# Optimization experiments

Measured on AMD Instinct MI355X. Metric: run time of the kernel, lower is better.

Reference implementation:

```python
import jax, jax.numpy as jnp
import numpy as np
from jax import lax

B, H, W, C = 16, 256, 256, 1
LOC_C = 31            # channels out of localization network
BN_EPS = 1e-3         # Keras BatchNormalization default epsilon
NEG_SLOPE = 0.1       # LeakyReLU slope


def _conv_relu(x, k, b):
    y = lax.conv_general_dilated(x, k, (1, 1), 'SAME',
                                 dimension_numbers=('NHWC', 'HWIO', 'NHWC'))
    return jax.nn.relu(y + b)


def _maxpool2(x):
    return lax.reduce_window(x, -jnp.inf, lax.max, (1, 2, 2, 1), (1, 2, 2, 1), 'VALID')


def _resize_nearest(x, out_h, out_w):
    # tf.image.resize(..., method='nearest') with half-pixel centers
    b, h, w, c = x.shape
    ih = jnp.floor((jnp.arange(out_h) + 0.5) * h / out_h).astype(jnp.int32)
    iw = jnp.floor((jnp.arange(out_w) + 0.5) * w / out_w).astype(jnp.int32)
    return x[:, ih][:, :, iw]


def _generate_grid(theta, height, width):
    # base grid in [-1, 1], x varies along width, y along height
    xs = jnp.arange(width, dtype=jnp.float32) / (width - 1) * 2.0 - 1.0
    ys = jnp.arange(height, dtype=jnp.float32) / (height - 1) * 2.0 - 1.0
    gx, gy = jnp.meshgrid(xs, ys)                      # (H, W)
    grid = jnp.stack([gx, gy], axis=-1).reshape(height * width, 2)  # (HW, 2)
    th = theta.reshape(-1, 2, 3)
    A = th[:, :, :2]                                   # (B, 2, 2)
    t = th[:, :, 2]                                    # (B, 2)
    # NOTE: source does grid @ A (not A @ grid) -- replicate exactly
    tg = jnp.einsum('nc,bcd->bnd', grid, A) + t[:, None, :]
    return tg.reshape(-1, height, width, 2)


def _sampler(img, grid):
    b, h, w, c = img.shape
    x = 0.5 * ((grid[..., 0] + 1.0) * (w - 1))
    y = 0.5 * ((grid[..., 1] + 1.0) * (h - 1))
    x0 = jnp.floor(x); x1 = x0 + 1.0
    y0 = jnp.floor(y); y1 = y0 + 1.0
    x0 = jnp.clip(x0, 0.0, w - 1.0); x1 = jnp.clip(x1, 0.0, w - 1.0)
    y0 = jnp.clip(y0, 0.0, h - 1.0); y1 = jnp.clip(y1, 0.0, h - 1.0)
    wa = (x1 - x) * (y1 - y)
    wb = (x1 - x) * (y - y0)
    wc = (x - x0) * (y1 - y)
    wd = (x - x0) * (y - y0)
    xi0 = x0.astype(jnp.int32); xi1 = x1.astype(jnp.int32)
    yi0 = y0.astype(jnp.int32); yi1 = y1.astype(jnp.int32)
    img_flat = img.reshape(b, h * w, c)

    def gather(yi, xi):
        idx = (yi * w + xi).reshape(b, h * w, 1)       # (B, HW, 1)
        return jnp.take_along_axis(img_flat, idx, axis=1).reshape(b, h, w, c)

    Ia = gather(yi0, xi0)
    Ib = gather(yi1, xi0)
    Ic = gather(yi0, xi1)
    Id = gather(yi1, xi1)
    return (wa[..., None] * Ia + wb[..., None] * Ib
            + wc[..., None] * Ic + wd[..., None] * Id)


def setup_inputs() -> dict:
    key = jax.random.key(0)
    ks = jax.random.split(key, 16)
    s = 0.05
    feat = (H // 8) * (W // 8) * LOC_C  # 31744 flattened localization features
    return {
        'x': jax.random.normal(ks[0], (B, H, W, C), jnp.float32),
        'conv1_k': jax.random.normal(ks[1], (3, 3, C, 8), jnp.float32) * s,
        'conv1_b': jnp.zeros((8,), jnp.float32),
        'conv2_k': jax.random.normal(ks[2], (3, 3, 8, 16), jnp.float32) * s,
        'conv2_b': jnp.zeros((16,), jnp.float32),
        'conv3_k': jax.random.normal(ks[3], (3, 3, 16, LOC_C), jnp.float32) * s,
        'conv3_b': jnp.zeros((LOC_C,), jnp.float32),
        'bn_gamma': 1.0 + 0.1 * jax.random.normal(ks[4], (feat,), jnp.float32),
        'bn_beta': 0.1 * jax.random.normal(ks[5], (feat,), jnp.float32),
        'bn_mean': jnp.zeros((feat,), jnp.float32),
        'bn_var': jnp.ones((feat,), jnp.float32),
        'd1_k': jax.random.normal(ks[6], (feat, 64), jnp.float32) * 0.01,
        'd1_b': jnp.zeros((64,), jnp.float32),
        'd2_k': jax.random.normal(ks[7], (64, 96), jnp.float32) * s,
        'd2_b': jnp.zeros((96,), jnp.float32),
        'd3_k': jax.random.normal(ks[8], (96, 6), jnp.float32) * 0.01,
        'd3_b': jnp.array([1, 0, 0, 0, 1, 0], jnp.float32),
    }


def reference(x, conv1_k, conv1_b, conv2_k, conv2_b, conv3_k, conv3_b,
              bn_gamma, bn_beta, bn_mean, bn_var,
              d1_k, d1_b, d2_k, d2_b, d3_k, d3_b):
    # localization network: (conv-relu, pool) x3 -> (B, H/8, W/8, 31)
    xi = _maxpool2(_conv_relu(x, conv1_k, conv1_b))
    xi = _maxpool2(_conv_relu(xi, conv2_k, conv2_b))
    x_intermediate = _maxpool2(_conv_relu(xi, conv3_k, conv3_b))
    # transformation parameter network (BN in inference mode, dropout = identity)
    f = x_intermediate.reshape(x.shape[0], -1)
    f = (f - bn_mean) * jax.lax.rsqrt(bn_var + BN_EPS) * bn_gamma + bn_beta
    f = jax.nn.relu(f @ d1_k + d1_b)
    f = jax.nn.relu(f @ d2_k + d2_b)
    theta = f @ d3_k + d3_b                            # (B, 6)
    grid = _generate_grid(theta, H, W)                 # (B, H, W, 2)
    loc_up = _resize_nearest(x_intermediate, H, W)     # (B, H, W, 31)
    xc = jnp.concatenate([x, loc_up], axis=-1)         # (B, H, W, 32)
    out = _sampler(xc, grid)
    return jnp.where(out >= 0, out, NEG_SLOPE * out)
```

## Files before the change

### kernel.cpp

```cpp
#include <hip/hip_runtime.h>


#define NEG_SLOPE 0.1f
#define BN_EPS 1e-3f

typedef float vfloat4 __attribute__((ext_vector_type(4)));

__device__ __forceinline__ void fma4v(float pv, float4 wq, float* __restrict__ acc) {
    acc[0] = fmaf(pv, wq.x, acc[0]);
    acc[1] = fmaf(pv, wq.y, acc[1]);
    acc[2] = fmaf(pv, wq.z, acc[2]);
    acc[3] = fmaf(pv, wq.w, acc[3]);
}

__global__ __launch_bounds__(256) void st_conv1(const float* __restrict__ x,
                                                const float* __restrict__ w,
                                                const float* __restrict__ bias,
                                                float* __restrict__ Ap,
                                                float* __restrict__ Bp) {
    int idx = blockIdx.x * 256 + threadIdx.x;
    int px = idx & 127, py = (idx >> 7) & 127, b = idx >> 14;
    const float* xb = x + b * 65536;
    int iy0 = 2 * py - 1, ix0 = 2 * px - 1;
    float p[16];
#pragma unroll
    for (int r = 0; r < 4; ++r) {
        int iy = iy0 + r;
        bool oky = (iy >= 0) && (iy < 256);
#pragma unroll
        for (int cc = 0; cc < 4; ++cc) {
            int ix = ix0 + cc;
            bool ok = oky && (ix >= 0) && (ix < 256);
            p[r * 4 + cc] = ok ? xb[iy * 256 + ix] : 0.0f;
        }
    }
    float m[8];
#pragma unroll
    for (int co = 0; co < 8; ++co) m[co] = -1e30f;
#pragma unroll
    for (int oy = 0; oy < 2; ++oy)
#pragma unroll
        for (int ox = 0; ox < 2; ++ox) {
            float acc[8];
#pragma unroll
            for (int co = 0; co < 8; ++co) acc[co] = 0.0f;
#pragma unroll
            for (int ky = 0; ky < 3; ++ky)
#pragma unroll
                for (int kx = 0; kx < 3; ++kx) {
                    float pv = p[(oy + ky) * 4 + (ox + kx)];
                    const float* wr = w + (ky * 3 + kx) * 8;
#pragma unroll
                    for (int co = 0; co < 8; ++co)
                        acc[co] = fmaf(pv, wr[co], acc[co]);
                }
#pragma unroll
            for (int co = 0; co < 8; ++co) m[co] = fmaxf(m[co], acc[co]);
        }
    float4 o0, o1;
    float r0 = m[0] + bias[0], r1 = m[1] + bias[1], r2 = m[2] + bias[2], r3 = m[3] + bias[3];
    float r4 = m[4] + bias[4], r5 = m[5] + bias[5], r6 = m[6] + bias[6], r7 = m[7] + bias[7];
    o0.x = r0 > 0.f ? r0 : 0.f; o0.y = r1 > 0.f ? r1 : 0.f;
    o0.z = r2 > 0.f ? r2 : 0.f; o0.w = r3 > 0.f ? r3 : 0.f;
    o1.x = r4 > 0.f ? r4 : 0.f; o1.y = r5 > 0.f ? r5 : 0.f;
    o1.z = r6 > 0.f ? r6 : 0.f; o1.w = r7 > 0.f ? r7 : 0.f;
    float* o = Ap + ((b * 130 + py + 1) * 130 + (px + 1)) * 8;
    *(float4*)o = o0;
    *(float4*)(o + 4) = o1;

    const float4 z4 = {0.f, 0.f, 0.f, 0.f};
    if (idx < 8256) {
        int bb = idx / 516, t = idx - bb * 516;
        int iy, ix;
        if (t < 130)      { iy = 0;       ix = t; }
        else if (t < 260) { iy = 129;     ix = t - 130; }
        else if (t < 388) { iy = t - 259; ix = 0; }
        else              { iy = t - 387; ix = 129; }
        float* d = Ap + ((bb * 130 + iy) * 130 + ix) * 8;
        *(float4*)d = z4; *(float4*)(d + 4) = z4;
    } else if (idx < 12416) {
        int r = idx - 8256;
        int bb = r / 260, t = r - bb * 260;
        int iy, ix;
        if (t < 66)       { iy = 0;       ix = t; }
        else if (t < 132) { iy = 65;      ix = t - 66; }
        else if (t < 196) { iy = t - 131; ix = 0; }
        else              { iy = t - 195; ix = 65; }
        float* d = Bp + ((bb * 66 + iy) * 66 + ix) * 16;
        *(float4*)d = z4; *(float4*)(d + 4) = z4;
        *(float4*)(d + 8) = z4; *(float4*)(d + 12) = z4;
    }
}

__global__ __launch_bounds__(256) void st_conv2(const float* __restrict__ Ap,
                                                const float* __restrict__ w,
                                                const float* __restrict__ bias,
                                                float* __restrict__ Bp) {
    __shared__ __align__(16) float wlds[1152];
    int t = threadIdx.x;
    for (int i = t; i < 1152; i += 256) wlds[i] = w[i];
    __syncthreads();
    int lane = t & 63;
    int wv = __builtin_amdgcn_readfirstlane(t >> 6);
    int cobase = wv * 4;
    int pixel = blockIdx.x * 64 + lane;
    int px = pixel & 63, py = (pixel >> 6) & 63, b = pixel >> 12;
    const float* Ab = Ap + b * 135200;
    int rowbase = (2 * py) * 130 + 2 * px;
    float acc[4][4];
#pragma unroll
    for (int pos = 0; pos < 4; ++pos)
#pragma unroll
        for (int c = 0; c < 4; ++c) acc[pos][c] = 0.0f;

#pragma unroll
    for (int ciq = 0; ciq < 2; ++ciq) {
        float ps[64];
#pragma unroll
        for (int r = 0; r < 4; ++r)
#pragma unroll
            for (int cc = 0; cc < 4; ++cc) {
                float4 v = *(const float4*)(Ab + (rowbase + r * 130 + cc) * 8 + ciq * 4);
                int cell = r * 4 + cc;
                ps[cell * 4 + 0] = v.x; ps[cell * 4 + 1] = v.y;
                ps[cell * 4 + 2] = v.z; ps[cell * 4 + 3] = v.w;
            }
#pragma unroll
        for (int ky = 0; ky < 3; ++ky)
#pragma unroll
            for (int kx = 0; kx < 3; ++kx) {
                int tap = ky * 3 + kx;
#pragma unroll
                for (int comp = 0; comp < 4; ++comp) {
                    float4 wq = *(const float4*)&wlds[((tap * 8 + ciq * 4 + comp) << 4) + cobase];
#pragma unroll
                    for (int oy = 0; oy < 2; ++oy)
#pragma unroll
                        for (int ox = 0; ox < 2; ++ox) {
                            float pv = ps[((oy + ky) * 4 + (ox + kx)) * 4 + comp];
                            fma4v(pv, wq, acc[oy * 2 + ox]);
                        }
                }
            }
    }
    float4 o;
    float* oc = (float*)&o;
#pragma unroll
    for (int c = 0; c < 4; ++c) {
        float m = fmaxf(fmaxf(acc[0][c], acc[1][c]), fmaxf(acc[2][c], acc[3][c]));
        m += bias[cobase + c];
        oc[c] = m > 0.0f ? m : 0.0f;
    }
    *(float4*)(Bp + ((b * 66 + py + 1) * 66 + (px + 1)) * 16 + cobase) = o;
}

__global__ __launch_bounds__(256) void st_conv3p(const float* __restrict__ Bp,
                                                 const float* __restrict__ w,
                                                 const float* __restrict__ bias,
                                                 const float* __restrict__ gamma,
                                                 const float* __restrict__ beta,
                                                 const float* __restrict__ mean,
                                                 const float* __restrict__ var,
                                                 float* __restrict__ xip,
                                                 float* __restrict__ fprime) {
    __shared__ __align__(16) float wlds[9 * 16 * 32];
    int t = threadIdx.x;
    for (int i = t; i < 4464; i += 256) {
        int tapci = i / 31;
        int co = i - tapci * 31;
        wlds[(tapci << 5) + co] = w[i];
    }
    __syncthreads();
    int lane = t & 63;
    int wv = __builtin_amdgcn_readfirstlane(t >> 6);
    int quad = blockIdx.y * 4 + wv;
    int cobase = quad * 4;
    if (cobase > 27) cobase = 27;
    int pixel = blockIdx.x * 64 + lane;
    int b = pixel >> 10;
    int cell = pixel & 1023;
    int ppy = cell >> 5, ppx = cell & 31;
    const float* Bb = Bp + b * 69696;
    int rowbase = (2 * ppy) * 66 + 2 * ppx;
    float acc[4][4];
#pragma unroll
    for (int pos = 0; pos < 4; ++pos)
#pragma unroll
        for (int c = 0; c < 4; ++c) acc[pos][c] = 0.0f;

#pragma unroll 2
    for (int ciq = 0; ciq < 4; ++ciq) {
        float ps[64];
#pragma unroll
        for (int r = 0; r < 4; ++r)
#pragma unroll
            for (int cc = 0; cc < 4; ++cc) {
                float4 v = *(const float4*)(Bb + (rowbase + r * 66 + cc) * 16 + ciq * 4);
                int cell2 = r * 4 + cc;
                ps[cell2 * 4 + 0] = v.x; ps[cell2 * 4 + 1] = v.y;
                ps[cell2 * 4 + 2] = v.z; ps[cell2 * 4 + 3] = v.w;
            }
#pragma unroll
        for (int ky = 0; ky < 3; ++ky)
#pragma unroll
            for (int kx = 0; kx < 3; ++kx) {
                int tap = ky * 3 + kx;
#pragma unroll
                for (int comp = 0; comp < 4; ++comp) {
                    float4 wq = *(const float4*)&wlds[((tap * 16 + ciq * 4 + comp) << 5) + cobase];
#pragma unroll
                    for (int oy = 0; oy < 2; ++oy)
#pragma unroll
                        for (int ox = 0; ox < 2; ++ox) {
                            float pv = ps[((oy + ky) * 4 + (ox + kx)) * 4 + comp];
                            fma4v(pv, wq, acc[oy * 2 + ox]);
                        }
                }
            }
    }
    float* xcell = xip + (b << 15) + (cell << 5) + 1 + cobase;
#pragma unroll
    for (int c = 0; c < 4; ++c) {
        float m = fmaxf(fmaxf(acc[0][c], acc[1][c]), fmaxf(acc[2][c], acc[3][c]));
        m += bias[cobase + c];
        float v = m > 0.0f ? m : 0.0f;
        xcell[c] = v;
        int j = cell * 31 + cobase + c;
        float sc = gamma[j] * rsqrtf(var[j] + BN_EPS);
        fprime[j * 16 + b] = (v - mean[j]) * sc + beta[j];
    }
}

__global__ __launch_bounds__(256) void st_d1(const float* __restrict__ fp,
                                             const float* __restrict__ k1,
                                             float* __restrict__ partial) {
    int t = threadIdx.x, s = blockIdx.x;
    int o = t & 63;
    int sub = t >> 6;
    int subu = __builtin_amdgcn_readfirstlane(sub);
    int j0 = s * 64 + subu * 16;
    float acc[16];
#pragma unroll
    for (int b = 0; b < 16; ++b) acc[b] = 0.0f;
#pragma unroll 4
    for (int jj = 0; jj < 16; ++jj) {
        int j = j0 + jj;
        float kv = k1[j * 64 + o];
        const float* fpj = fp + j * 16;
#pragma unroll
        for (int b = 0; b < 16; ++b)
            acc[b] = fmaf(fpj[b], kv, acc[b]);
    }
    __shared__ float red[4][16][64];
#pragma unroll
    for (int b = 0; b < 16; ++b) red[sub][b][o] = acc[b];
    __syncthreads();
    if (sub == 0) {
#pragma unroll
        for (int b = 0; b < 16; ++b) {
            float v = red[0][b][o] + red[1][b][o] + red[2][b][o] + red[3][b][o];
            partial[(s * 64 + o) * 16 + b] = v;
        }
    }
}

__global__ __launch_bounds__(256) void st_d1b(const float* __restrict__ partial,
                                              const float* __restrict__ bias,
                                              float* __restrict__ h1) {
    int gid = blockIdx.x * 256 + threadIdx.x;
    int o = gid >> 4, b = gid & 15;
    float s = 0.0f;
#pragma unroll 8
    for (int sl = 0; sl < 496; ++sl) s += partial[(sl * 64 + o) * 16 + b];
    s += bias[o];
    h1[b * 64 + o] = s > 0.0f ? s : 0.0f;
}

__global__ __launch_bounds__(128) void st_theta(const float* __restrict__ h1,
                                                const float* __restrict__ k2,
                                                const float* __restrict__ b2,
                                                const float* __restrict__ k3,
                                                const float* __restrict__ b3,
                                                float* __restrict__ theta) {
    int b = blockIdx.x, t = threadIdx.x;
    __shared__ float h2[96];
    if (t < 96) {
        float s = b2[t];
        for (int i = 0; i < 64; ++i) s = fmaf(h1[b * 64 + i], k2[i * 96 + t], s);
        h2[t] = s > 0.0f ? s : 0.0f;
    }
    __syncthreads();
    if (t < 6) {
        float s = b3[t];
        for (int i = 0; i < 96; ++i) s = fmaf(h2[i], k3[i * 6 + t], s);
        theta[b * 6 + t] = s;
    }
}

__global__ __launch_bounds__(256) void st_sample(const float* __restrict__ x,
                                                 const float* __restrict__ xip,
                                                 const float* __restrict__ theta,
                                                 float* __restrict__ out) {
    int gid = blockIdx.x * 256 + threadIdx.x;
    int q = gid & 3;
    int pix = gid >> 2;
    int ow = pix & 255, oh = (pix >> 8) & 255;
    int b = __builtin_amdgcn_readfirstlane(blockIdx.x >> 10);

    const float* th = theta + b * 6;
    float t0 = th[0], t1 = th[1], t2 = th[2], t3 = th[3], t4 = th[4], t5 = th[5];
    float gx = (float)ow * (2.0f / 255.0f) - 1.0f;
    float gy = (float)oh * (2.0f / 255.0f) - 1.0f;
    float sx = gx * t0 + gy * t3 + t2;
    float sy = gx * t1 + gy * t4 + t5;
    float xf = 0.5f * ((sx + 1.0f) * 255.0f);
    float yf = 0.5f * ((sy + 1.0f) * 255.0f);
    float x0 = floorf(xf), y0 = floorf(yf);
    float x1 = x0 + 1.0f, y1 = y0 + 1.0f;
    x0 = fminf(fmaxf(x0, 0.0f), 255.0f);
    x1 = fminf(fmaxf(x1, 0.0f), 255.0f);
    y0 = fminf(fmaxf(y0, 0.0f), 255.0f);
    y1 = fminf(fmaxf(y1, 0.0f), 255.0f);
    float wa = (x1 - xf) * (y1 - yf);
    float wb = (x1 - xf) * (yf - y0);
    float wc = (xf - x0) * (y1 - yf);
    float wd = (xf - x0) * (yf - y0);
    int xi0 = (int)x0, xi1 = (int)x1, yi0 = (int)y0, yi1 = (int)y1;

    const float* cellbase = xip + (b << 15);
    int off = q * 8;
    const float* pa = cellbase + ((((yi0 >> 3) << 5) + (xi0 >> 3)) << 5) + off;
    const float* pb = cellbase + ((((yi1 >> 3) << 5) + (xi0 >> 3)) << 5) + off;
    const float* pc = cellbase + ((((yi0 >> 3) << 5) + (xi1 >> 3)) << 5) + off;
    const float* pd = cellbase + ((((yi1 >> 3) << 5) + (xi1 >> 3)) << 5) + off;

    float r[8];
#pragma unroll
    for (int k = 0; k < 2; ++k) {
        float4 va = *(const float4*)(pa + 4 * k);
        float4 vb = *(const float4*)(pb + 4 * k);
        float4 vc = *(const float4*)(pc + 4 * k);
        float4 vd = *(const float4*)(pd + 4 * k);
        r[4 * k]     = fmaf(wa, va.x, fmaf(wb, vb.x, fmaf(wc, vc.x, wd * vd.x)));
        r[4 * k + 1] = fmaf(wa, va.y, fmaf(wb, vb.y, fmaf(wc, vc.y, wd * vd.y)));
        r[4 * k + 2] = fmaf(wa, va.z, fmaf(wb, vb.z, fmaf(wc, vc.z, wd * vd.z)));
        r[4 * k + 3] = fmaf(wa, va.w, fmaf(wb, vb.w, fmaf(wc, vc.w, wd * vd.w)));
    }
    if (q == 0) {
        const float* xb = x + b * 65536;
        float Ia = xb[yi0 * 256 + xi0];
        float Ib = xb[yi1 * 256 + xi0];
        float Ic = xb[yi0 * 256 + xi1];
        float Id = xb[yi1 * 256 + xi1];
        r[0] = fmaf(wa, Ia, fmaf(wb, Ib, fmaf(wc, Ic, wd * Id)));
    }
#pragma unroll
    for (int i = 0; i < 8; ++i) r[i] = r[i] >= 0.0f ? r[i] : NEG_SLOPE * r[i];

    float* ob = out + pix * 32 + off;
    vfloat4 v0 = {r[0], r[1], r[2], r[3]};
    vfloat4 v1 = {r[4], r[5], r[6], r[7]};
    __builtin_nontemporal_store(v0, (vfloat4*)ob);
    __builtin_nontemporal_store(v1, (vfloat4*)(ob + 4));
}

extern "C" void kernel_launch(void* const* d_in, const int* in_sizes, int n_in,
                              void* d_out, int out_size, void* d_ws, size_t ws_size,
                              hipStream_t stream) {
    const float* x     = (const float*)d_in[0];
    const float* c1k   = (const float*)d_in[1];
    const float* c1b   = (const float*)d_in[2];
    const float* c2k   = (const float*)d_in[3];
    const float* c2b   = (const float*)d_in[4];
    const float* c3k   = (const float*)d_in[5];
    const float* c3b   = (const float*)d_in[6];
    const float* gamma = (const float*)d_in[7];
    const float* beta  = (const float*)d_in[8];
    const float* mean  = (const float*)d_in[9];
    const float* var   = (const float*)d_in[10];
    const float* d1k   = (const float*)d_in[11];
    const float* d1b   = (const float*)d_in[12];
    const float* d2k   = (const float*)d_in[13];
    const float* d2b   = (const float*)d_in[14];
    const float* d3k   = (const float*)d_in[15];
    const float* d3b   = (const float*)d_in[16];
    float* out = (float*)d_out;
    float* ws  = (float*)d_ws;

    float* Ap      = ws;
    float* Bp      = ws + 2163200;
    float* xip     = ws;
    float* fprime  = ws + 524288;
    float* partial = ws + 3278336;
    float* h1      = ws + 3786240;
    float* theta   = ws + 3787264;

    st_conv1<<<1024, 256, 0, stream>>>(x, c1k, c1b, Ap, Bp);
    st_conv2<<<1024, 256, 0, stream>>>(Ap, c2k, c2b, Bp);
    st_conv3p<<<dim3(256, 2), 256, 0, stream>>>(Bp, c3k, c3b, gamma, beta,
                                                mean, var, xip, fprime);
    st_d1<<<496, 256, 0, stream>>>(fprime, d1k, partial);
    st_d1b<<<4, 256, 0, stream>>>(partial, d1b, h1);
    st_theta<<<16, 128, 0, stream>>>(h1, d2k, d2b, d3k, d3b, theta);
    st_sample<<<16384, 256, 0, stream>>>(x, xip, theta, out);
}
```

Measured before the change: 263.3 us.

## Split conv2/conv3 input channels across wave halves and fuse dense head kernels

In conv2 and conv3, each wave's two 32-lane halves now take different input-channel groups for the same pixels, and the partial sums are combined with a cross-half shuffle. This doubles the grid size and halves each thread's serial work, which should raise parallelism and occupancy for these small conv layers. The d1 reduction and the d2/d3 theta kernels are merged into one kernel, removing a launch and an intermediate buffer. The cost is that half the lanes sit idle during the epilogue and the shuffle adds work.

```diff
diff --git a/kernel.cpp b/kernel.cpp
--- a/kernel.cpp
+++ b/kernel.cpp
@@ -101,9 +101,10 @@
     for (int i = t; i < 1152; i += 256) wlds[i] = w[i];
     __syncthreads();
     int lane = t & 63;
+    int ciq = lane >> 5;
     int wv = __builtin_amdgcn_readfirstlane(t >> 6);
     int cobase = wv * 4;
-    int pixel = blockIdx.x * 64 + lane;
+    int pixel = blockIdx.x * 32 + (lane & 31);
     int px = pixel & 63, py = (pixel >> 6) & 63, b = pixel >> 12;
     const float* Ab = Ap + b * 135200;
     int rowbase = (2 * py) * 130 + 2 * px;
@@ -113,45 +114,49 @@
 #pragma unroll
         for (int c = 0; c < 4; ++c) acc[pos][c] = 0.0f;
 
-#pragma unroll
-    for (int ciq = 0; ciq < 2; ++ciq) {
-        float ps[64];
-#pragma unroll
-        for (int r = 0; r < 4; ++r)
-#pragma unroll
-            for (int cc = 0; cc < 4; ++cc) {
-                float4 v = *(const float4*)(Ab + (rowbase + r * 130 + cc) * 8 + ciq * 4);
-                int cell = r * 4 + cc;
-                ps[cell * 4 + 0] = v.x; ps[cell * 4 + 1] = v.y;
-                ps[cell * 4 + 2] = v.z; ps[cell * 4 + 3] = v.w;
+    float ps[64];
+#pragma unroll
+    for (int r = 0; r < 4; ++r)
+#pragma unroll
+        for (int cc = 0; cc < 4; ++cc) {
+            float4 v = *(const float4*)(Ab + (rowbase + r * 130 + cc) * 8 + ciq * 4);
+            int cell = r * 4 + cc;
+            ps[cell * 4 + 0] = v.x; ps[cell * 4 + 1] = v.y;
+            ps[cell * 4 + 2] = v.z; ps[cell * 4 + 3] = v.w;
+        }
+#pragma unroll
+    for (int ky = 0; ky < 3; ++ky)
+#pragma unroll
+        for (int kx = 0; kx < 3; ++kx) {
+            int tap = ky * 3 + kx;
+#pragma unroll
+            for (int comp = 0; comp < 4; ++comp) {
+                float4 wq = *(const float4*)&wlds[((tap * 8 + ciq * 4 + comp) << 4) + cobase];
+#pragma unroll
+                for (int oy = 0; oy < 2; ++oy)
+#pragma unroll
+                    for (int ox = 0; ox < 2; ++ox) {
+                        float pv = ps[((oy + ky) * 4 + (ox + kx)) * 4 + comp];
+                        fma4v(pv, wq, acc[oy * 2 + ox]);
+                    }
             }
-#pragma unroll
-        for (int ky = 0; ky < 3; ++ky)
-#pragma unroll
-            for (int kx = 0; kx < 3; ++kx) {
-                int tap = ky * 3 + kx;
-#pragma unroll
-                for (int comp = 0; comp < 4; ++comp) {
-                    float4 wq = *(const float4*)&wlds[((tap * 8 + ciq * 4 + comp) << 4) + cobase];
-#pragma unroll
-                    for (int oy = 0; oy < 2; ++oy)
-#pragma unroll
-                        for (int ox = 0; ox < 2; ++ox) {
-                            float pv = ps[((oy + ky) * 4 + (ox + kx)) * 4 + comp];
-                            fma4v(pv, wq, acc[oy * 2 + ox]);
-                        }
-                }
-            }
-    }
-    float4 o;
-    float* oc = (float*)&o;
-#pragma unroll
-    for (int c = 0; c < 4; ++c) {
-        float m = fmaxf(fmaxf(acc[0][c], acc[1][c]), fmaxf(acc[2][c], acc[3][c]));
-        m += bias[cobase + c];
-        oc[c] = m > 0.0f ? m : 0.0f;
-    }
-    *(float4*)(Bp + ((b * 66 + py + 1) * 66 + (px + 1)) * 16 + cobase) = o;
+        }
+#pragma unroll
+    for (int pos = 0; pos < 4; ++pos)
+#pragma unroll
+        for (int c = 0; c < 4; ++c)
+            acc[pos][c] += __shfl_down(acc[pos][c], 32, 64);
+    if (ciq == 0) {
+        float4 o;
+        float* oc = (float*)&o;
+#pragma unroll
+        for (int c = 0; c < 4; ++c) {
+            float m = fmaxf(fmaxf(acc[0][c], acc[1][c]), fmaxf(acc[2][c], acc[3][c]));
+            m += bias[cobase + c];
+            oc[c] = m > 0.0f ? m : 0.0f;
+        }
+        *(float4*)(Bp + ((b * 66 + py + 1) * 66 + (px + 1)) * 16 + cobase) = o;
+    }
 }
 
 __global__ __launch_bounds__(256) void st_conv3p(const float* __restrict__ Bp,
@@ -172,11 +177,12 @@
     }
     __syncthreads();
     int lane = t & 63;
+    int half = lane >> 5;
     int wv = __builtin_amdgcn_readfirstlane(t >> 6);
     int quad = blockIdx.y * 4 + wv;
     int cobase = quad * 4;
     if (cobase > 27) cobase = 27;
-    int pixel = blockIdx.x * 64 + lane;
+    int pixel = blockIdx.x * 32 + (lane & 31);
     int b = pixel >> 10;
     int cell = pixel & 1023;
     int ppy = cell >> 5, ppx = cell & 31;
@@ -188,8 +194,9 @@
 #pragma unroll
         for (int c = 0; c < 4; ++c) acc[pos][c] = 0.0f;
 
-#pragma unroll 2
-    for (int ciq = 0; ciq < 4; ++ciq) {
+#pragma unroll
+    for (int ii = 0; ii < 2; ++ii) {
+        int ciq = half * 2 + ii;
         float ps[64];
 #pragma unroll
         for (int r = 0; r < 4; ++r)
@@ -218,16 +225,23 @@
                 }
             }
     }
-    float* xcell = xip + (b << 15) + (cell << 5) + 1 + cobase;
-#pragma unroll
-    for (int c = 0; c < 4; ++c) {
-        float m = fmaxf(fmaxf(acc[0][c], acc[1][c]), fmaxf(acc[2][c], acc[3][c]));
-        m += bias[cobase + c];
-        float v = m > 0.0f ? m : 0.0f;
-        xcell[c] = v;
-        int j = cell * 31 + cobase + c;
-        float sc = gamma[j] * rsqrtf(var[j] + BN_EPS);
-        fprime[j * 16 + b] = (v - mean[j]) * sc + beta[j];
+#pragma unroll
+    for (int pos = 0; pos < 4; ++pos)
+#pragma unroll
+        for (int c = 0; c < 4; ++c)
+            acc[pos][c] += __shfl_down(acc[pos][c], 32, 64);
+    if (half == 0) {
+        float* xcell = xip + (b << 15) + (cell << 5) + 1 + cobase;
+#pragma unroll
+        for (int c = 0; c < 4; ++c) {
+            float m = fmaxf(fmaxf(acc[0][c], acc[1][c]), fmaxf(acc[2][c], acc[3][c]));
+            m += bias[cobase + c];
+            float v = m > 0.0f ? m : 0.0f;
+            xcell[c] = v;
+            int j = cell * 31 + cobase + c;
+            float sc = gamma[j] * rsqrtf(var[j] + BN_EPS);
+            fprime[j * 16 + b] = (v - mean[j]) * sc + beta[j];
+        }
     }
 }
 
@@ -264,29 +278,27 @@
     }
 }
 
-__global__ __launch_bounds__(256) void st_d1b(const float* __restrict__ partial,
-                                              const float* __restrict__ bias,
-                                              float* __restrict__ h1) {
-    int gid = blockIdx.x * 256 + threadIdx.x;
-    int o = gid >> 4, b = gid & 15;
-    float s = 0.0f;
+__global__ __launch_bounds__(128) void st_head(const float* __restrict__ partial,
+                                               const float* __restrict__ b1,
+                                               const float* __restrict__ k2,
+                                               const float* __restrict__ b2,
+                                               const float* __restrict__ k3,
+                                               const float* __restrict__ b3,
+                                               float* __restrict__ theta) {
+    int b = blockIdx.x, t = threadIdx.x;
+    __shared__ float h1[64];
+    __shared__ float h2[96];
+    if (t < 64) {
+        float s = 0.0f;
 #pragma unroll 8
-    for (int sl = 0; sl < 496; ++sl) s += partial[(sl * 64 + o) * 16 + b];
-    s += bias[o];
-    h1[b * 64 + o] = s > 0.0f ? s : 0.0f;
-}
-
-__global__ __launch_bounds__(128) void st_theta(const float* __restrict__ h1,
-                                                const float* __restrict__ k2,
-                                                const float* __restrict__ b2,
-                                                const float* __restrict__ k3,
-                                                const float* __restrict__ b3,
-                                                float* __restrict__ theta) {
-    int b = blockIdx.x, t = threadIdx.x;
-    __shared__ float h2[96];
+        for (int sl = 0; sl < 496; ++sl) s += partial[(sl * 64 + t) * 16 + b];
+        s += b1[t];
+        h1[t] = s > 0.0f ? s : 0.0f;
+    }
+    __syncthreads();
     if (t < 96) {
         float s = b2[t];
-        for (int i = 0; i < 64; ++i) s = fmaf(h1[b * 64 + i], k2[i * 96 + t], s);
+        for (int i = 0; i < 64; ++i) s = fmaf(h1[i], k2[i * 96 + t], s);
         h2[t] = s > 0.0f ? s : 0.0f;
     }
     __syncthreads();
@@ -392,15 +404,13 @@
     float* xip     = ws;
     float* fprime  = ws + 524288;
     float* partial = ws + 3278336;
-    float* h1      = ws + 3786240;
-    float* theta   = ws + 3787264;
+    float* theta   = ws + 3786240;
 
     st_conv1<<<1024, 256, 0, stream>>>(x, c1k, c1b, Ap, Bp);
-    st_conv2<<<1024, 256, 0, stream>>>(Ap, c2k, c2b, Bp);
-    st_conv3p<<<dim3(256, 2), 256, 0, stream>>>(Bp, c3k, c3b, gamma, beta,
+    st_conv2<<<2048, 256, 0, stream>>>(Ap, c2k, c2b, Bp);
+    st_conv3p<<<dim3(512, 2), 256, 0, stream>>>(Bp, c3k, c3b, gamma, beta,
                                                 mean, var, xip, fprime);
     st_d1<<<496, 256, 0, stream>>>(fprime, d1k, partial);
-    st_d1b<<<4, 256, 0, stream>>>(partial, d1b, h1);
-    st_theta<<<16, 128, 0, stream>>>(h1, d2k, d2b, d3k, d3b, theta);
+    st_head<<<16, 128, 0, stream>>>(partial, d1b, d2k, d2b, d3k, d3b, theta);
     st_sample<<<16384, 256, 0, stream>>>(x, xip, theta, out);
 }
```

Result: slower. 271.6 us (+3.1%).
